# Performance work log

Measured on AMD Instinct MI355X. Metric: run time of the kernel, lower is better.

Reference implementation:

```python
import jax, jax.numpy as jnp
import numpy as np

NEG = -1e9

def conv1x1(x, w, b):
    # x: [B,C,H,W], w: [O,C], b: [O]
    return jnp.einsum('bchw,oc->bohw', x, w) + b[None, :, None, None]


def setup_inputs() -> dict:
    key = jax.random.key(0)
    ks = jax.random.split(key, 12)
    B, C, H, W = 4, 512, 96, 96
    Cr = min(8, C // 8)  # = 8
    s = lambda fan: 1.0 / np.sqrt(fan)
    inp = {
        'x':   jax.random.normal(ks[0], (B, C, H, W), dtype=jnp.float32),
        'w_h': jax.random.normal(ks[1], (Cr, C), dtype=jnp.float32) * s(C),
        'b_h': jax.random.normal(ks[2], (Cr,), dtype=jnp.float32) * s(C),
        'w_w': jax.random.normal(ks[3], (Cr, C), dtype=jnp.float32) * s(C),
        'b_w': jax.random.normal(ks[4], (Cr,), dtype=jnp.float32) * s(C),
        'w_c': jax.random.normal(ks[5], (C, C), dtype=jnp.float32) * s(C),
        'b_c': jax.random.normal(ks[6], (C,), dtype=jnp.float32) * s(C),
        'w_o': jax.random.normal(ks[7], (C, C), dtype=jnp.float32) * s(C),
        'b_o': jax.random.normal(ks[8], (C,), dtype=jnp.float32) * s(C),
        # alpha/beta/gamma are nn.Parameter(zeros(1)); use small nonzero values
        # so all branches contribute to output/gradients.
        'alpha': jax.random.normal(ks[9], (1,), dtype=jnp.float32) * 0.1,
        'beta':  jax.random.normal(ks[10], (1,), dtype=jnp.float32) * 0.1,
        'gamma': jax.random.normal(ks[11], (1,), dtype=jnp.float32) * 0.1,
    }
    return inp


def reference(x, w_h, b_h, w_w, b_w, w_c, b_c, w_o, b_o, alpha, beta, gamma):
    B, C, H, W = x.shape
    f_hei = conv1x1(x, w_h, b_h)              # [B,Cr,H,W]
    Cr = f_hei.shape[1]
    # Faithful replication of torch permute/contiguous/view sequence
    # (the .view(B*W,-1,H) after permute reinterprets the (H,Cr) layout as (Cr,H)).
    f_h = f_hei.transpose(0, 3, 2, 1).reshape(B * W, Cr, H).transpose(0, 2, 1)  # [B*W,H,Cr]
    f_w = f_hei.transpose(0, 2, 1, 3).reshape(B * H, Cr, W).transpose(0, 2, 1)  # [B*H,W,Cr]
    f_wid = conv1x1(x, w_w, b_w)              # [B,Cr,H,W]
    ff_h = f_wid.transpose(0, 3, 1, 2).reshape(B * W, Cr, H)  # [B*W,Cr,H]
    ff_w = f_wid.transpose(0, 2, 1, 3).reshape(B * H, Cr, W)  # [B*H,Cr,W]
    # channel attention branch
    f_ch = conv1x1(x, w_c, b_c)               # [B,C,H,W]
    f_c = f_ch.reshape(B, C, H * W)           # [B,C,HW]
    ff_c = f_ch.transpose(0, 2, 3, 1).reshape(B, H * W, C)    # [B,HW,C]
    aff_c = jax.nn.softmax(jnp.matmul(f_c, ff_c), axis=2)     # [B,C,C]
    out_C = jnp.matmul(ff_c, aff_c).reshape(B, C, H, W)       # torch .view reinterpretation
    # axial (criss-cross) attention with masked concat-softmax
    E_h = jnp.matmul(f_h, ff_h)               # [B*W,H,H]
    E_h = E_h + (jnp.eye(H, dtype=x.dtype) * NEG)[None, :, :]
    E_h = E_h.reshape(B, W, H, H).transpose(0, 2, 1, 3)       # [B,H,W,H]
    E_w = jnp.matmul(f_w, ff_w).reshape(B, H, W, W)           # [B,H,W,W]
    concate = jax.nn.softmax(jnp.concatenate([E_h, E_w], axis=3), axis=3)  # [B,H,W,H+W]
    h_att = concate[:, :, :, :H].transpose(0, 2, 1, 3).reshape(B * W, H, H)
    w_att = concate[:, :, :, H:].reshape(B * H, W, W)
    f_cha = conv1x1(x, w_o, b_o)              # [B,C,H,W]
    P_H = f_cha.transpose(0, 3, 1, 2).reshape(B * W, C, H)
    P_W = f_cha.transpose(0, 2, 1, 3).reshape(B * H, C, W)
    out_H = jnp.matmul(P_H, h_att.transpose(0, 2, 1)).reshape(B, W, C, H).transpose(0, 2, 3, 1)
    out_W = jnp.matmul(P_W, w_att.transpose(0, 2, 1)).reshape(B, H, C, W).transpose(0, 2, 1, 3)
    return x + alpha * out_H + beta * out_W + gamma * out_C
```

## Files before the change

kernel.cpp:

```cpp
#include <hip/hip_runtime.h>

typedef __attribute__((ext_vector_type(8))) short short8;
typedef __attribute__((ext_vector_type(4))) float f32x4;
typedef __attribute__((ext_vector_type(4))) unsigned short us4;
typedef unsigned short u16;

#define kB 4
#define kC 512
#define kCr 8
#define kH 96
#define kW 96
#define kHW 9216
#define kCHW 4718592
#define NEGV -1e9f

__device__ __forceinline__ u16 f2b(float f) {
  union { float f; unsigned u; } v; v.f = f;
  unsigned r = v.u + 0x7fff + ((v.u >> 16) & 1);
  return (u16)(r >> 16);
}
__device__ __forceinline__ float b2f(u16 h) {
  union { unsigned u; float f; } v; v.u = ((unsigned)h) << 16;
  return v.f;
}
#define MFMA(a, b, c) __builtin_amdgcn_mfma_f32_16x16x32_bf16(a, b, c, 0, 0, 0)

__global__ __launch_bounds__(256) void k_cvt_T(const float* __restrict__ in,
                                               u16* __restrict__ out,
                                               int R, int C) {
  const float* ib = in + (size_t)blockIdx.z * R * C;
  u16* ob = out + (size_t)blockIdx.z * R * C;
  int c0 = blockIdx.x * 64, r0 = blockIdx.y * 64;
  __shared__ u16 T[64][68];
  int tid = threadIdx.x;
#pragma unroll
  for (int p = 0; p < 4; p++) {
    int ch = tid + p * 256;
    int i = ch >> 4, seg = ch & 15;
    f32x4 v = *(const f32x4*)&ib[(size_t)(r0 + i) * C + c0 + seg * 4];
    T[i][seg*4+0] = f2b(v[0]); T[i][seg*4+1] = f2b(v[1]);
    T[i][seg*4+2] = f2b(v[2]); T[i][seg*4+3] = f2b(v[3]);
  }
  __syncthreads();
#pragma unroll
  for (int p = 0; p < 4; p++) {
    int ch = tid + p * 256;
    int j = ch >> 4, seg = ch & 15;
    us4 o;
#pragma unroll
    for (int e = 0; e < 4; e++) o[e] = T[seg*4+e][j];
    *(us4*)&ob[(size_t)(c0 + j) * R + r0 + seg * 4] = o;
  }
}

__global__ __launch_bounds__(256) void k_trT_bf(const u16* __restrict__ in,
                                                u16* __restrict__ out,
                                                int R, int C) {
  const u16* ib = in + (size_t)blockIdx.z * R * C;
  u16* ob = out + (size_t)blockIdx.z * R * C;
  int c0 = blockIdx.x * 64, r0 = blockIdx.y * 64;
  __shared__ u16 T[64][68];
  int tid = threadIdx.x;
#pragma unroll
  for (int p = 0; p < 4; p++) {
    int ch = tid + p * 256;
    int i = ch >> 4, seg = ch & 15;
    us4 v = *(const us4*)&ib[(size_t)(r0 + i) * C + c0 + seg * 4];
    T[i][seg*4+0] = v[0]; T[i][seg*4+1] = v[1];
    T[i][seg*4+2] = v[2]; T[i][seg*4+3] = v[3];
  }
  __syncthreads();
#pragma unroll
  for (int p = 0; p < 4; p++) {
    int ch = tid + p * 256;
    int j = ch >> 4, seg = ch & 15;
    us4 o;
#pragma unroll
    for (int e = 0; e < 4; e++) o[e] = T[seg*4+e][j];
    *(us4*)&ob[(size_t)(c0 + j) * R + r0 + seg * 4] = o;
  }
}

__global__ __launch_bounds__(256) void k_conv16(
    const float* __restrict__ wh, const float* __restrict__ bh,
    const float* __restrict__ ww, const float* __restrict__ bw,
    const u16* __restrict__ XT, u16* __restrict__ Out) {
  __shared__ u16 As[16][520];
  __shared__ float bias_s[16];
  int tid = threadIdx.x;
#pragma unroll
  for (int p = 0; p < 4; p++) {
    int ch = tid + p * 256;
    int r = ch >> 6, seg = ch & 63;
    const float* src = (r < 8) ? &wh[r * 512 + seg * 8] : &ww[(r - 8) * 512 + seg * 8];
    f32x4 v0 = *(const f32x4*)src;
    f32x4 v1 = *(const f32x4*)(src + 4);
    short8 sv;
    sv[0]=f2b(v0[0]); sv[1]=f2b(v0[1]); sv[2]=f2b(v0[2]); sv[3]=f2b(v0[3]);
    sv[4]=f2b(v1[0]); sv[5]=f2b(v1[1]); sv[6]=f2b(v1[2]); sv[7]=f2b(v1[3]);
    *(short8*)&As[r][seg * 8] = sv;
  }
  if (tid < 16) bias_s[tid] = (tid < 8) ? bh[tid] : bw[tid - 8];
  __syncthreads();
  int b = blockIdx.y;
  int nb = blockIdx.x * 128 + (tid >> 6) * 32;
  int lane = tid & 63;
  int lr = lane & 15, lg = lane >> 4;
  const u16* Bb = XT + (size_t)b * kCHW;
  f32x4 acc[2] = {};
#pragma unroll 4
  for (int k0 = 0; k0 < 512; k0 += 32) {
    short8 a = *(const short8*)&As[lr][k0 + lg * 8];
    short8 b0 = *(const short8*)&Bb[(size_t)(nb + lr) * 512 + k0 + lg * 8];
    short8 b1 = *(const short8*)&Bb[(size_t)(nb + 16 + lr) * 512 + k0 + lg * 8];
    acc[0] = MFMA(a, b0, acc[0]);
    acc[1] = MFMA(a, b1, acc[1]);
  }
#pragma unroll
  for (int q = 0; q < 2; q++)
#pragma unroll
    for (int r = 0; r < 4; r++) {
      int m = lg * 4 + r;
      Out[((size_t)b * 16 + m) * kHW + nb + q * 16 + lr] = f2b(acc[q][r] + bias_s[m]);
    }
}

__global__ __launch_bounds__(256) void k_gemm_conv(
    const float* __restrict__ A, const u16* __restrict__ BT,
    const float* __restrict__ bias, u16* __restrict__ Out) {
  int b = blockIdx.z;
  int bm = blockIdx.y * 128;
  int bn = blockIdx.x * 128;
  const u16* Bb = BT + (size_t)b * kCHW;
  __shared__ u16 As[128][72];
  __shared__ u16 Bs[128][72];
  int tid = threadIdx.x;
  int lane = tid & 63, wv = tid >> 6;
  int wr = (wv >> 1) * 64, wc = (wv & 1) * 64;
  int lr = lane & 15, lg = lane >> 4;
  f32x4 acc[4][4] = {};
  for (int k0 = 0; k0 < kC; k0 += 64) {
#pragma unroll
    for (int p = 0; p < 4; p++) {
      int ch = tid + p * 256;
      int row = ch >> 3, seg = ch & 7;
      const float* src = &A[(size_t)(bm + row) * 512 + k0 + seg * 8];
      f32x4 v0 = *(const f32x4*)src;
      f32x4 v1 = *(const f32x4*)(src + 4);
      short8 sv;
      sv[0]=f2b(v0[0]); sv[1]=f2b(v0[1]); sv[2]=f2b(v0[2]); sv[3]=f2b(v0[3]);
      sv[4]=f2b(v1[0]); sv[5]=f2b(v1[1]); sv[6]=f2b(v1[2]); sv[7]=f2b(v1[3]);
      *(short8*)&As[row][seg*8] = sv;
      *(short8*)&Bs[row][seg*8] = *(const short8*)&Bb[(size_t)(bn+row)*512 + k0 + seg*8];
    }
    __syncthreads();
#pragma unroll
    for (int ks = 0; ks < 2; ks++) {
      short8 av[4], bv[4];
#pragma unroll
      for (int m = 0; m < 4; m++) av[m] = *(const short8*)&As[wr + m*16 + lr][ks*32 + lg*8];
#pragma unroll
      for (int n = 0; n < 4; n++) bv[n] = *(const short8*)&Bs[wc + n*16 + lr][ks*32 + lg*8];
#pragma unroll
      for (int m = 0; m < 4; m++)
#pragma unroll
        for (int n = 0; n < 4; n++)
          acc[m][n] = MFMA(av[m], bv[n], acc[m][n]);
    }
    __syncthreads();
  }
  u16* Ob = Out + (size_t)b * kCHW;
#pragma unroll
  for (int m = 0; m < 4; m++)
#pragma unroll
    for (int r = 0; r < 4; r++) {
      int o = bm + wr + m*16 + lg*4 + r;
      float bv_ = bias[o];
#pragma unroll
      for (int n = 0; n < 4; n++)
        Ob[(size_t)o * kHW + bn + wc + n*16 + lr] = f2b(acc[m][n][r] + bv_);
    }
}

__global__ __launch_bounds__(256) void k_gram_sk(const u16* __restrict__ F,
                                                float* __restrict__ part) {
  int z = blockIdx.z;
  int b = z & 3, s = z >> 2;
  int bm = blockIdx.y * 128, bn = blockIdx.x * 128;
  const u16* Fb = F + (size_t)b * kCHW;
  __shared__ u16 As[128][72];
  __shared__ u16 Bs[128][72];
  int tid = threadIdx.x;
  int lane = tid & 63, wv = tid >> 6;
  int wr = (wv >> 1) * 64, wc = (wv & 1) * 64;
  int lr = lane & 15, lg = lane >> 4;
  f32x4 acc[4][4] = {};
  int kbeg = s * 1152;
  for (int k0 = kbeg; k0 < kbeg + 1152; k0 += 64) {
#pragma unroll
    for (int p = 0; p < 4; p++) {
      int ch = tid + p * 256;
      int row = ch >> 3, seg = ch & 7;
      *(short8*)&As[row][seg*8] = *(const short8*)&Fb[(size_t)(bm+row)*kHW + k0 + seg*8];
      *(short8*)&Bs[row][seg*8] = *(const short8*)&Fb[(size_t)(bn+row)*kHW + k0 + seg*8];
    }
    __syncthreads();
#pragma unroll
    for (int ks = 0; ks < 2; ks++) {
      short8 av[4], bv[4];
#pragma unroll
      for (int m = 0; m < 4; m++) av[m] = *(const short8*)&As[wr + m*16 + lr][ks*32 + lg*8];
#pragma unroll
      for (int n = 0; n < 4; n++) bv[n] = *(const short8*)&Bs[wc + n*16 + lr][ks*32 + lg*8];
#pragma unroll
      for (int m = 0; m < 4; m++)
#pragma unroll
        for (int n = 0; n < 4; n++)
          acc[m][n] = MFMA(av[m], bv[n], acc[m][n]);
    }
    __syncthreads();
  }
  float* Pb = part + ((size_t)(s * 4 + b)) * 262144;
#pragma unroll
  for (int m = 0; m < 4; m++)
#pragma unroll
    for (int r = 0; r < 4; r++) {
      int i = bm + wr + m*16 + lg*4 + r;
#pragma unroll
      for (int n = 0; n < 4; n++)
        Pb[(size_t)i * 512 + bn + wc + n*16 + lr] = acc[m][n][r];
    }
}

__global__ __launch_bounds__(256) void k_softmax512r(const float* __restrict__ part,
                                                     float* __restrict__ gramN) {
  int b = blockIdx.x >> 9, i = blockIdx.x & 511;
  int tid = threadIdx.x;
  float v0 = 0.f, v1 = 0.f;
#pragma unroll
  for (int s = 0; s < 8; s++) {
    const float* P = part + ((size_t)(s * 4 + b) * 512 + i) * 512;
    v0 += P[tid];
    v1 += P[tid + 256];
  }
  int wid = tid >> 6, lane = tid & 63;
  float m = fmaxf(v0, v1);
#pragma unroll
  for (int o = 32; o >= 1; o >>= 1) m = fmaxf(m, __shfl_xor(m, o));
  __shared__ float redm[4], reds[4];
  if (lane == 0) redm[wid] = m;
  __syncthreads();
  m = fmaxf(fmaxf(redm[0], redm[1]), fmaxf(redm[2], redm[3]));
  float e0 = expf(v0 - m), e1 = expf(v1 - m);
  float s = e0 + e1;
#pragma unroll
  for (int o = 32; o >= 1; o >>= 1) s += __shfl_xor(s, o);
  if (lane == 0) reds[wid] = s;
  __syncthreads();
  s = reds[0] + reds[1] + reds[2] + reds[3];
  float inv = 1.0f / s;
  float* R = gramN + ((size_t)b * 512 + i) * 512;
  R[tid] = e0 * inv;
  R[tid + 256] = e1 * inv;
}

__global__ __launch_bounds__(256) void k_outc(
    const u16* __restrict__ AT, const u16* __restrict__ Bt,
    const float* __restrict__ gamma, u16* __restrict__ Out) {
  int b = blockIdx.z;
  int bm = blockIdx.y * 128;
  int bn = blockIdx.x * 128;
  const u16* Ab = AT + (size_t)b * kCHW;
  const u16* Bb = Bt + (size_t)b * 262144;
  __shared__ u16 As[128][72];
  __shared__ u16 Bs[128][72];
  int tid = threadIdx.x;
  int lane = tid & 63, wv = tid >> 6;
  int wr = (wv >> 1) * 64, wc = (wv & 1) * 64;
  int lr = lane & 15, lg = lane >> 4;
  f32x4 acc[4][4] = {};
  for (int k0 = 0; k0 < kC; k0 += 64) {
#pragma unroll
    for (int p = 0; p < 4; p++) {
      int ch = tid + p * 256;
      int row = ch >> 3, seg = ch & 7;
      *(short8*)&As[row][seg*8] = *(const short8*)&Ab[(size_t)(bm+row)*512 + k0 + seg*8];
      *(short8*)&Bs[row][seg*8] = *(const short8*)&Bb[(size_t)(bn+row)*512 + k0 + seg*8];
    }
    __syncthreads();
#pragma unroll
    for (int ks = 0; ks < 2; ks++) {
      short8 av[4], bv[4];
#pragma unroll
      for (int m = 0; m < 4; m++) av[m] = *(const short8*)&As[wr + m*16 + lr][ks*32 + lg*8];
#pragma unroll
      for (int n = 0; n < 4; n++) bv[n] = *(const short8*)&Bs[wc + n*16 + lr][ks*32 + lg*8];
#pragma unroll
      for (int m = 0; m < 4; m++)
#pragma unroll
        for (int n = 0; n < 4; n++)
          acc[m][n] = MFMA(av[m], bv[n], acc[m][n]);
    }
    __syncthreads();
  }
  float g = *gamma;
  u16* Ob = Out + (size_t)b * kCHW;
#pragma unroll
  for (int m = 0; m < 4; m++)
#pragma unroll
    for (int r = 0; r < 4; r++) {
      int mm = bm + wr + m*16 + lg*4 + r;
#pragma unroll
      for (int n = 0; n < 4; n++)
        Ob[(size_t)mm * 512 + bn + wc + n*16 + lr] = f2b(g * acc[m][n][r]);
    }
}

__global__ __launch_bounds__(256) void k_eh(
    const u16* __restrict__ fhw, u16* __restrict__ Ccat) {
  int b = blockIdx.x / kW, w = blockIdx.x % kW;
  __shared__ float fh[kH][kCr];
  __shared__ float fw[kCr][kH];
  int tid = threadIdx.x;
  for (int l = tid; l < kH * kCr; l += 256) {
    int i = l >> 3, c = l & 7;
    fh[i][c] = b2f(fhw[((size_t)b * 16 + (i & 7)) * kHW + (c * 12 + (i >> 3)) * kW + w]);
    int c2 = l / kH, j = l % kH;
    fw[c2][j] = b2f(fhw[((size_t)b * 16 + 8 + c2) * kHW + j * kW + w]);
  }
  __syncthreads();
  for (int t = tid; t < kH * kH; t += 256) {
    int i = t / kH, j = t % kH;
    float e = 0.f;
#pragma unroll
    for (int c = 0; c < kCr; c++) e += fh[i][c] * fw[c][j];
    if (i == j) e += NEGV;
    Ccat[(((size_t)b * kH + i) * kW + w) * 192 + j] = f2b(e);
  }
}

__global__ __launch_bounds__(256) void k_ew(
    const u16* __restrict__ fhw, u16* __restrict__ Ccat) {
  int b = blockIdx.x / kH, h = blockIdx.x % kH;
  __shared__ float fh2[kCr][kW];
  __shared__ float fw2[kCr][kW];
  int tid = threadIdx.x;
  for (int l = tid; l < kCr * kW; l += 256) {
    int c = l / kW, w = l % kW;
    fh2[c][w] = b2f(fhw[((size_t)b * 16 + c) * kHW + h * kW + w]);
    fw2[c][w] = b2f(fhw[((size_t)b * 16 + 8 + c) * kHW + h * kW + w]);
  }
  __syncthreads();
  for (int t = tid; t < kW * kW; t += 256) {
    int w = t / kW, j = t % kW;
    float e = 0.f;
#pragma unroll
    for (int c = 0; c < kCr; c++) e += fh2[c][w] * fw2[c][j];
    Ccat[(((size_t)b * kH + h) * kW + w) * 192 + 96 + j] = f2b(e);
  }
}

__global__ __launch_bounds__(256) void k_softmax192(u16* __restrict__ Ccat) {
  int r = blockIdx.x * 4 + (threadIdx.x >> 6);
  int lane = threadIdx.x & 63;
  u16* R = Ccat + (size_t)r * 192;
  float a = b2f(R[lane]), b = b2f(R[lane + 64]), c = b2f(R[lane + 128]);
  float m = fmaxf(a, fmaxf(b, c));
#pragma unroll
  for (int o = 32; o >= 1; o >>= 1) m = fmaxf(m, __shfl_xor(m, o));
  float ea = expf(a - m), eb = expf(b - m), ec = expf(c - m);
  float s = ea + eb + ec;
#pragma unroll
  for (int o = 32; o >= 1; o >>= 1) s += __shfl_xor(s, o);
  float inv = 1.0f / s;
  R[lane] = f2b(ea * inv);
  R[lane + 64] = f2b(eb * inv);
  R[lane + 128] = f2b(ec * inv);
}

__global__ __launch_bounds__(256) void k_tr_plane(const u16* __restrict__ in,
                                                  u16* __restrict__ out) {
  size_t pl = blockIdx.x;
  const u16* ib = in + pl * 9216;
  u16* ob = out + pl * 9216;
  __shared__ u16 T[96][100];
  int tid = threadIdx.x;
  for (int ch = tid; ch < 96 * 24; ch += 256) {
    int i = ch / 24, seg = ch % 24;
    *(us4*)&T[i][seg*4] = *(const us4*)&ib[i*96 + seg*4];
  }
  __syncthreads();
  for (int ch = tid; ch < 96 * 24; ch += 256) {
    int j = ch / 24, seg = ch % 24;
    us4 o;
#pragma unroll
    for (int e = 0; e < 4; e++) o[e] = T[seg*4+e][j];
    *(us4*)&ob[j*96 + seg*4] = o;
  }
}

__global__ __launch_bounds__(512) void k_final_h(
    const u16* __restrict__ AT,
    const u16* __restrict__ att,
    const float* __restrict__ alpha,
    u16* __restrict__ OutHT) {
  int b = blockIdx.x / 96, w = blockIdx.x % 96;
  __shared__ u16 Bs[96][104];
  int tid = threadIdx.x;
  for (int ch = tid; ch < 1152; ch += 512) {
    int h = ch / 12, seg = ch % 12;
    *(short8*)&Bs[h][seg*8] =
        *(const short8*)&att[(((size_t)b*96 + h)*96 + w)*192 + seg*8];
  }
  __syncthreads();
  int lane = tid & 63, wv = tid >> 6;
  int lr = lane & 15, lg = lane >> 4;
  int c0 = wv * 64;
  const u16* Ab = AT + ((size_t)b*512 + c0)*kHW + w*96;
  f32x4 acc[4][6] = {};
#pragma unroll
  for (int ks = 0; ks < 3; ks++) {
    short8 av[4];
#pragma unroll
    for (int m = 0; m < 4; m++)
      av[m] = *(const short8*)&Ab[(size_t)(m*16 + lr)*kHW + ks*32 + lg*8];
#pragma unroll
    for (int n = 0; n < 6; n++) {
      short8 bv = *(const short8*)&Bs[n*16 + lr][ks*32 + lg*8];
#pragma unroll
      for (int m = 0; m < 4; m++) acc[m][n] = MFMA(av[m], bv, acc[m][n]);
    }
  }
  float al = *alpha;
  u16* Ob = OutHT + ((size_t)b*512 + c0)*kHW + w*96;
#pragma unroll
  for (int m = 0; m < 4; m++)
#pragma unroll
    for (int r = 0; r < 4; r++) {
      size_t crow = (size_t)(m*16 + lg*4 + r) * kHW;
#pragma unroll
      for (int n = 0; n < 6; n++)
        Ob[crow + n*16 + lr] = f2b(al * acc[m][n][r]);
    }
}

__global__ __launch_bounds__(512) void k_final_w(
    const u16* __restrict__ A,
    const u16* __restrict__ att,
    const float* __restrict__ beta,
    u16* __restrict__ OutW) {
  int b = blockIdx.x / 96, h = blockIdx.x % 96;
  __shared__ u16 Bs[96][104];
  int tid = threadIdx.x;
  for (int ch = tid; ch < 1152; ch += 512) {
    int wr_ = ch / 12, seg = ch % 12;
    *(short8*)&Bs[wr_][seg*8] =
        *(const short8*)&att[(((size_t)b*96 + h)*96 + wr_)*192 + 96 + seg*8];
  }
  __syncthreads();
  int lane = tid & 63, wv = tid >> 6;
  int lr = lane & 15, lg = lane >> 4;
  int c0 = wv * 64;
  const u16* Ab = A + ((size_t)b*512 + c0)*kHW + h*96;
  f32x4 acc[4][6] = {};
#pragma unroll
  for (int ks = 0; ks < 3; ks++) {
    short8 av[4];
#pragma unroll
    for (int m = 0; m < 4; m++)
      av[m] = *(const short8*)&Ab[(size_t)(m*16 + lr)*kHW + ks*32 + lg*8];
#pragma unroll
    for (int n = 0; n < 6; n++) {
      short8 bv = *(const short8*)&Bs[n*16 + lr][ks*32 + lg*8];
#pragma unroll
      for (int m = 0; m < 4; m++) acc[m][n] = MFMA(av[m], bv, acc[m][n]);
    }
  }
  float be = *beta;
  u16* Ob = OutW + ((size_t)b*512 + c0)*kHW + h*96;
#pragma unroll
  for (int m = 0; m < 4; m++)
#pragma unroll
    for (int r = 0; r < 4; r++) {
      size_t crow = (size_t)(m*16 + lg*4 + r) * kHW;
#pragma unroll
      for (int n = 0; n < 6; n++)
        Ob[crow + n*16 + lr] = f2b(be * acc[m][n][r]);
    }
}

__global__ __launch_bounds__(256) void k_merge(
    const float* __restrict__ x, const u16* __restrict__ OutC,
    const u16* __restrict__ OutW, const u16* __restrict__ HT,
    float* __restrict__ out) {
  size_t pl = blockIdx.x;
  const u16* hb = HT + pl * 9216;
  __shared__ u16 T[96][100];
  int tid = threadIdx.x;
  for (int ch = tid; ch < 96 * 24; ch += 256) {
    int i = ch / 24, seg = ch % 24;
    *(us4*)&T[i][seg*4] = *(const us4*)&hb[i*96 + seg*4];
  }
  __syncthreads();
  const float* xb = x + pl * 9216;
  const u16* cb = OutC + pl * 9216;
  const u16* wb = OutW + pl * 9216;
  float* ob = out + pl * 9216;
  for (int ch = tid; ch < 2304; ch += 256) {
    int i4 = ch * 4;
    int h = i4 / 96, w = i4 % 96;
    f32x4 xv = *(const f32x4*)&xb[i4];
    us4 cv = *(const us4*)&cb[i4];
    us4 wv = *(const us4*)&wb[i4];
    f32x4 o;
#pragma unroll
    for (int e = 0; e < 4; e++)
      o[e] = xv[e] + b2f(cv[e]) + b2f(wv[e]) + b2f(T[w + e][h]);
    *(f32x4*)&ob[i4] = o;
  }
}

extern "C" void kernel_launch(void* const* d_in, const int* in_sizes, int n_in,
                              void* d_out, int out_size, void* d_ws, size_t ws_size,
                              hipStream_t stream) {
  const float* x     = (const float*)d_in[0];
  const float* w_h   = (const float*)d_in[1];
  const float* b_h   = (const float*)d_in[2];
  const float* w_w   = (const float*)d_in[3];
  const float* b_w   = (const float*)d_in[4];
  const float* w_c   = (const float*)d_in[5];
  const float* b_c   = (const float*)d_in[6];
  const float* w_o   = (const float*)d_in[7];
  const float* b_o   = (const float*)d_in[8];
  const float* alpha = (const float*)d_in[9];
  const float* beta  = (const float*)d_in[10];
  const float* gamma = (const float*)d_in[11];
  float* out = (float*)d_out;

  const size_t R = 37748736;
  char* p = (char*)d_ws;
  u16*   xbfT   = (u16*)(p);
  float* part   = (float*)(p);
  u16*   f_chaT = (u16*)(p);
  u16*   outW   = (u16*)(p);
  u16*   f_ch   = (u16*)(p + R);
  u16*   outC   = (u16*)(p + R);
  u16*   f_chT  = (u16*)(p + 2 * R);
  u16*   outHT  = (u16*)(p + 2 * R);
  u16*   f_cha  = (u16*)(p + 3 * R);
  u16*   fhw    = (u16*)(p + 4 * R);
  char*  F      = p + 4 * R + 2359296;
  float* gramN  = (float*)F;
  u16*   affT   = (u16*)(F + 4194304);
  u16*   ccat   = (u16*)F;

  k_cvt_T<<<dim3(144, 8, 4), 256, 0, stream>>>(x, xbfT, 512, 9216);
  k_conv16<<<dim3(72, 4), 256, 0, stream>>>(w_h, b_h, w_w, b_w, xbfT, fhw);
  k_gemm_conv<<<dim3(72, 4, 4), 256, 0, stream>>>(w_c, xbfT, b_c, f_ch);
  k_gemm_conv<<<dim3(72, 4, 4), 256, 0, stream>>>(w_o, xbfT, b_o, f_cha);
  k_trT_bf<<<dim3(144, 8, 4), 256, 0, stream>>>(f_ch, f_chT, 512, 9216);
  k_gram_sk<<<dim3(4, 4, 32), 256, 0, stream>>>(f_ch, part);
  k_softmax512r<<<2048, 256, 0, stream>>>(part, gramN);
  k_cvt_T<<<dim3(8, 8, 4), 256, 0, stream>>>(gramN, affT, 512, 512);
  k_outc<<<dim3(4, 72, 4), 256, 0, stream>>>(f_chT, affT, gamma, outC);
  k_eh<<<384, 256, 0, stream>>>(fhw, ccat);
  k_ew<<<384, 256, 0, stream>>>(fhw, ccat);
  k_softmax192<<<9216, 256, 0, stream>>>(ccat);
  k_tr_plane<<<2048, 256, 0, stream>>>(f_cha, f_chaT);
  k_final_h<<<384, 512, 0, stream>>>(f_chaT, ccat, alpha, outHT);
  k_final_w<<<384, 512, 0, stream>>>(f_cha, ccat, beta, outW);
  k_merge<<<2048, 256, 0, stream>>>(x, outC, outW, outHT, out);
}
```

Before: 342.1 us.

## Double-buffer GEMMs with direct global-to-LDS loads, swizzled LDS, and merged conv launch

The three MFMA GEMM kernels (1x1 conv, Gram, out_C) now stage tiles into double-buffered LDS with global_load_lds, so the next K-slab is fetched while the current one is computed. LDS tiles use an XOR swizzle instead of padding to avoid bank conflicts. The w_c/w_o weights are converted to bf16 once by a new small kernel, which lets the two conv GEMMs merge into one launch with a doubled M grid and drops the per-tile fp32-to-bf16 conversion. This costs double the LDS per block, which may lower occupancy, and adds one extra tiny launch.

```diff
diff --git a/kernel.cpp b/kernel.cpp
--- a/kernel.cpp
+++ b/kernel.cpp
@@ -25,6 +25,12 @@
 }
 #define MFMA(a, b, c) __builtin_amdgcn_mfma_f32_16x16x32_bf16(a, b, c, 0, 0, 0)
 
+__device__ __forceinline__ void gl16(const u16* g, u16* l) {
+  __builtin_amdgcn_global_load_lds(
+      (const __attribute__((address_space(1))) void*)g,
+      (__attribute__((address_space(3))) void*)l, 16, 0, 0);
+}
+
 __global__ __launch_bounds__(256) void k_cvt_T(const float* __restrict__ in,
                                                u16* __restrict__ out,
                                                int R, int C) {
@@ -79,6 +85,17 @@
     for (int e = 0; e < 4; e++) o[e] = T[seg*4+e][j];
     *(us4*)&ob[(size_t)(c0 + j) * R + r0 + seg * 4] = o;
   }
+}
+
+__global__ __launch_bounds__(256) void k_cvtw(const float* __restrict__ wc,
+                                              const float* __restrict__ wo,
+                                              u16* __restrict__ wco) {
+  int i = blockIdx.x * 256 + threadIdx.x;
+  const float* src = (i < 65536) ? &wc[(size_t)i * 4] : &wo[(size_t)(i - 65536) * 4];
+  f32x4 v = *(const f32x4*)src;
+  us4 o;
+  o[0] = f2b(v[0]); o[1] = f2b(v[1]); o[2] = f2b(v[2]); o[3] = f2b(v[3]);
+  ((us4*)wco)[i] = o;
 }
 
 __global__ __launch_bounds__(256) void k_conv16(
@@ -125,110 +142,152 @@
     }
 }
 
-__global__ __launch_bounds__(256) void k_gemm_conv(
-    const float* __restrict__ A, const u16* __restrict__ BT,
-    const float* __restrict__ bias, u16* __restrict__ Out) {
+#define GEMM_PROLOG()                                                      \
+  int tid = threadIdx.x;                                                   \
+  int lane = tid & 63, wv = tid >> 6;                                      \
+  int wr = (wv >> 1) * 64, wc = (wv & 1) * 64;                             \
+  int lr = lane & 15, lg = lane >> 4;                                      \
+  f32x4 acc[4][4] = {};
+
+#define STAGE(bufv, kk)                                                    \
+  {                                                                        \
+    _Pragma("unroll")                                                      \
+    for (int p = 0; p < 4; p++) {                                          \
+      int ch = tid + p * 256;                                              \
+      int row = ch >> 3, cc = ch & 7;                                      \
+      int sc = (cc ^ (row & 7)) * 8;                                       \
+      gl16(&Asrc[(size_t)(bm + row) * LDA + (kk) + sc], &As[bufv][row][cc * 8]); \
+      gl16(&Bsrc[(size_t)(bn + row) * LDB + (kk) + sc], &Bs[bufv][row][cc * 8]); \
+    }                                                                      \
+  }
+
+#define COMPUTE(bufv)                                                      \
+  {                                                                        \
+    _Pragma("unroll")                                                      \
+    for (int ks = 0; ks < 2; ks++) {                                       \
+      int ca = ((ks * 4 + lg) ^ (lr & 7)) * 8;                             \
+      short8 av[4], bv[4];                                                 \
+      _Pragma("unroll")                                                    \
+      for (int m = 0; m < 4; m++)                                          \
+        av[m] = *(const short8*)&As[bufv][wr + m * 16 + lr][ca];           \
+      _Pragma("unroll")                                                    \
+      for (int n = 0; n < 4; n++)                                          \
+        bv[n] = *(const short8*)&Bs[bufv][wc + n * 16 + lr][ca];           \
+      _Pragma("unroll")                                                    \
+      for (int m = 0; m < 4; m++)                                          \
+        _Pragma("unroll")                                                  \
+        for (int n = 0; n < 4; n++)                                        \
+          acc[m][n] = MFMA(av[m], bv[n], acc[m][n]);                       \
+    }                                                                      \
+  }
+
+__global__ __launch_bounds__(256) void k_gemm_conv2(
+    const u16* __restrict__ wco, const u16* __restrict__ BT,
+    const float* __restrict__ b_c, const float* __restrict__ b_o,
+    u16* __restrict__ f_ch, u16* __restrict__ f_cha) {
+  __shared__ u16 As[2][128][64];
+  __shared__ u16 Bs[2][128][64];
   int b = blockIdx.z;
   int bm = blockIdx.y * 128;
   int bn = blockIdx.x * 128;
-  const u16* Bb = BT + (size_t)b * kCHW;
-  __shared__ u16 As[128][72];
-  __shared__ u16 Bs[128][72];
-  int tid = threadIdx.x;
-  int lane = tid & 63, wv = tid >> 6;
-  int wr = (wv >> 1) * 64, wc = (wv & 1) * 64;
-  int lr = lane & 15, lg = lane >> 4;
-  f32x4 acc[4][4] = {};
-  for (int k0 = 0; k0 < kC; k0 += 64) {
-#pragma unroll
-    for (int p = 0; p < 4; p++) {
-      int ch = tid + p * 256;
-      int row = ch >> 3, seg = ch & 7;
-      const float* src = &A[(size_t)(bm + row) * 512 + k0 + seg * 8];
-      f32x4 v0 = *(const f32x4*)src;
-      f32x4 v1 = *(const f32x4*)(src + 4);
-      short8 sv;
-      sv[0]=f2b(v0[0]); sv[1]=f2b(v0[1]); sv[2]=f2b(v0[2]); sv[3]=f2b(v0[3]);
-      sv[4]=f2b(v1[0]); sv[5]=f2b(v1[1]); sv[6]=f2b(v1[2]); sv[7]=f2b(v1[3]);
-      *(short8*)&As[row][seg*8] = sv;
-      *(short8*)&Bs[row][seg*8] = *(const short8*)&Bb[(size_t)(bn+row)*512 + k0 + seg*8];
-    }
+  const u16* Asrc = wco;
+  const u16* Bsrc = BT + (size_t)b * kCHW;
+  const int LDA = 512, LDB = 512;
+  GEMM_PROLOG();
+  STAGE(0, 0);
+  __syncthreads();
+  int cur = 0;
+#pragma unroll 1
+  for (int t = 0; t < 7; t++) {
+    STAGE(cur ^ 1, (t + 1) * 64);
+    COMPUTE(cur);
     __syncthreads();
-#pragma unroll
-    for (int ks = 0; ks < 2; ks++) {
-      short8 av[4], bv[4];
-#pragma unroll
-      for (int m = 0; m < 4; m++) av[m] = *(const short8*)&As[wr + m*16 + lr][ks*32 + lg*8];
-#pragma unroll
-      for (int n = 0; n < 4; n++) bv[n] = *(const short8*)&Bs[wc + n*16 + lr][ks*32 + lg*8];
-#pragma unroll
-      for (int m = 0; m < 4; m++)
-#pragma unroll
-        for (int n = 0; n < 4; n++)
-          acc[m][n] = MFMA(av[m], bv[n], acc[m][n]);
-    }
-    __syncthreads();
-  }
-  u16* Ob = Out + (size_t)b * kCHW;
+    cur ^= 1;
+  }
+  COMPUTE(cur);
+  const float* biasp = (bm < 512) ? (b_c + bm) : (b_o + bm - 512);
+  u16* Ob = (bm < 512) ? (f_ch + (size_t)b * kCHW + (size_t)bm * kHW)
+                       : (f_cha + (size_t)b * kCHW + (size_t)(bm - 512) * kHW);
 #pragma unroll
   for (int m = 0; m < 4; m++)
 #pragma unroll
     for (int r = 0; r < 4; r++) {
-      int o = bm + wr + m*16 + lg*4 + r;
-      float bv_ = bias[o];
+      int ol = wr + m * 16 + lg * 4 + r;
+      float bv_ = biasp[ol];
 #pragma unroll
       for (int n = 0; n < 4; n++)
-        Ob[(size_t)o * kHW + bn + wc + n*16 + lr] = f2b(acc[m][n][r] + bv_);
+        Ob[(size_t)ol * kHW + bn + wc + n * 16 + lr] = f2b(acc[m][n][r] + bv_);
     }
 }
 
 __global__ __launch_bounds__(256) void k_gram_sk(const u16* __restrict__ F,
-                                                float* __restrict__ part) {
+                                                 float* __restrict__ part) {
+  __shared__ u16 As[2][128][64];
+  __shared__ u16 Bs[2][128][64];
   int z = blockIdx.z;
   int b = z & 3, s = z >> 2;
   int bm = blockIdx.y * 128, bn = blockIdx.x * 128;
-  const u16* Fb = F + (size_t)b * kCHW;
-  __shared__ u16 As[128][72];
-  __shared__ u16 Bs[128][72];
-  int tid = threadIdx.x;
-  int lane = tid & 63, wv = tid >> 6;
-  int wr = (wv >> 1) * 64, wc = (wv & 1) * 64;
-  int lr = lane & 15, lg = lane >> 4;
-  f32x4 acc[4][4] = {};
+  const u16* Asrc = F + (size_t)b * kCHW;
+  const u16* Bsrc = Asrc;
+  const int LDA = kHW, LDB = kHW;
   int kbeg = s * 1152;
-  for (int k0 = kbeg; k0 < kbeg + 1152; k0 += 64) {
-#pragma unroll
-    for (int p = 0; p < 4; p++) {
-      int ch = tid + p * 256;
-      int row = ch >> 3, seg = ch & 7;
-      *(short8*)&As[row][seg*8] = *(const short8*)&Fb[(size_t)(bm+row)*kHW + k0 + seg*8];
-      *(short8*)&Bs[row][seg*8] = *(const short8*)&Fb[(size_t)(bn+row)*kHW + k0 + seg*8];
-    }
+  GEMM_PROLOG();
+  STAGE(0, kbeg);
+  __syncthreads();
+  int cur = 0;
+#pragma unroll 1
+  for (int t = 0; t < 17; t++) {
+    STAGE(cur ^ 1, kbeg + (t + 1) * 64);
+    COMPUTE(cur);
     __syncthreads();
-#pragma unroll
-    for (int ks = 0; ks < 2; ks++) {
-      short8 av[4], bv[4];
-#pragma unroll
-      for (int m = 0; m < 4; m++) av[m] = *(const short8*)&As[wr + m*16 + lr][ks*32 + lg*8];
-#pragma unroll
-      for (int n = 0; n < 4; n++) bv[n] = *(const short8*)&Bs[wc + n*16 + lr][ks*32 + lg*8];
-#pragma unroll
-      for (int m = 0; m < 4; m++)
-#pragma unroll
-        for (int n = 0; n < 4; n++)
-          acc[m][n] = MFMA(av[m], bv[n], acc[m][n]);
-    }
+    cur ^= 1;
+  }
+  COMPUTE(cur);
+  float* Pb = part + ((size_t)(s * 4 + b)) * 262144;
+#pragma unroll
+  for (int m = 0; m < 4; m++)
+#pragma unroll
+    for (int r = 0; r < 4; r++) {
+      int i = bm + wr + m * 16 + lg * 4 + r;
+#pragma unroll
+      for (int n = 0; n < 4; n++)
+        Pb[(size_t)i * 512 + bn + wc + n * 16 + lr] = acc[m][n][r];
+    }
+}
+
+__global__ __launch_bounds__(256) void k_outc(
+    const u16* __restrict__ AT, const u16* __restrict__ Bt,
+    const float* __restrict__ gamma, u16* __restrict__ Out) {
+  __shared__ u16 As[2][128][64];
+  __shared__ u16 Bs[2][128][64];
+  int b = blockIdx.z;
+  int bm = blockIdx.y * 128;
+  int bn = blockIdx.x * 128;
+  const u16* Asrc = AT + (size_t)b * kCHW;
+  const u16* Bsrc = Bt + (size_t)b * 262144;
+  const int LDA = 512, LDB = 512;
+  GEMM_PROLOG();
+  STAGE(0, 0);
+  __syncthreads();
+  int cur = 0;
+#pragma unroll 1
+  for (int t = 0; t < 7; t++) {
+    STAGE(cur ^ 1, (t + 1) * 64);
+    COMPUTE(cur);
     __syncthreads();
-  }
-  float* Pb = part + ((size_t)(s * 4 + b)) * 262144;
+    cur ^= 1;
+  }
+  COMPUTE(cur);
+  float g = *gamma;
+  u16* Ob = Out + (size_t)b * kCHW;
 #pragma unroll
   for (int m = 0; m < 4; m++)
 #pragma unroll
     for (int r = 0; r < 4; r++) {
-      int i = bm + wr + m*16 + lg*4 + r;
+      int mm = bm + wr + m * 16 + lg * 4 + r;
 #pragma unroll
       for (int n = 0; n < 4; n++)
-        Pb[(size_t)i * 512 + bn + wc + n*16 + lr] = acc[m][n][r];
+        Ob[(size_t)mm * 512 + bn + wc + n * 16 + lr] = f2b(g * acc[m][n][r]);
     }
 }
 
@@ -262,58 +321,6 @@
   float* R = gramN + ((size_t)b * 512 + i) * 512;
   R[tid] = e0 * inv;
   R[tid + 256] = e1 * inv;
-}
-
-__global__ __launch_bounds__(256) void k_outc(
-    const u16* __restrict__ AT, const u16* __restrict__ Bt,
-    const float* __restrict__ gamma, u16* __restrict__ Out) {
-  int b = blockIdx.z;
-  int bm = blockIdx.y * 128;
-  int bn = blockIdx.x * 128;
-  const u16* Ab = AT + (size_t)b * kCHW;
-  const u16* Bb = Bt + (size_t)b * 262144;
-  __shared__ u16 As[128][72];
-  __shared__ u16 Bs[128][72];
-  int tid = threadIdx.x;
-  int lane = tid & 63, wv = tid >> 6;
-  int wr = (wv >> 1) * 64, wc = (wv & 1) * 64;
-  int lr = lane & 15, lg = lane >> 4;
-  f32x4 acc[4][4] = {};
-  for (int k0 = 0; k0 < kC; k0 += 64) {
-#pragma unroll
-    for (int p = 0; p < 4; p++) {
-      int ch = tid + p * 256;
-      int row = ch >> 3, seg = ch & 7;
-      *(short8*)&As[row][seg*8] = *(const short8*)&Ab[(size_t)(bm+row)*512 + k0 + seg*8];
-      *(short8*)&Bs[row][seg*8] = *(const short8*)&Bb[(size_t)(bn+row)*512 + k0 + seg*8];
-    }
-    __syncthreads();
-#pragma unroll
-    for (int ks = 0; ks < 2; ks++) {
-      short8 av[4], bv[4];
-#pragma unroll
-      for (int m = 0; m < 4; m++) av[m] = *(const short8*)&As[wr + m*16 + lr][ks*32 + lg*8];
-#pragma unroll
-      for (int n = 0; n < 4; n++) bv[n] = *(const short8*)&Bs[wc + n*16 + lr][ks*32 + lg*8];
-#pragma unroll
-      for (int m = 0; m < 4; m++)
-#pragma unroll
-        for (int n = 0; n < 4; n++)
-          acc[m][n] = MFMA(av[m], bv[n], acc[m][n]);
-    }
-    __syncthreads();
-  }
-  float g = *gamma;
-  u16* Ob = Out + (size_t)b * kCHW;
-#pragma unroll
-  for (int m = 0; m < 4; m++)
-#pragma unroll
-    for (int r = 0; r < 4; r++) {
-      int mm = bm + wr + m*16 + lg*4 + r;
-#pragma unroll
-      for (int n = 0; n < 4; n++)
-        Ob[(size_t)mm * 512 + bn + wc + n*16 + lr] = f2b(g * acc[m][n][r]);
-    }
 }
 
 __global__ __launch_bounds__(256) void k_eh(
@@ -553,11 +560,12 @@
   float* gramN  = (float*)F;
   u16*   affT   = (u16*)(F + 4194304);
   u16*   ccat   = (u16*)F;
+  u16*   wco    = (u16*)(F + 14155776);
 
   k_cvt_T<<<dim3(144, 8, 4), 256, 0, stream>>>(x, xbfT, 512, 9216);
+  k_cvtw<<<512, 256, 0, stream>>>(w_c, w_o, wco);
   k_conv16<<<dim3(72, 4), 256, 0, stream>>>(w_h, b_h, w_w, b_w, xbfT, fhw);
-  k_gemm_conv<<<dim3(72, 4, 4), 256, 0, stream>>>(w_c, xbfT, b_c, f_ch);
-  k_gemm_conv<<<dim3(72, 4, 4), 256, 0, stream>>>(w_o, xbfT, b_o, f_cha);
+  k_gemm_conv2<<<dim3(72, 8, 4), 256, 0, stream>>>(wco, xbfT, b_c, b_o, f_ch, f_cha);
   k_trT_bf<<<dim3(144, 8, 4), 256, 0, stream>>>(f_ch, f_chT, 512, 9216);
   k_gram_sk<<<dim3(4, 4, 32), 256, 0, stream>>>(f_ch, part);
   k_softmax512r<<<2048, 256, 0, stream>>>(part, gramN);
```

Result: faster. 310.7 us (-9.2%).
